# Kernel optimization log

Hardware: AMD Instinct MI355X
Metric: run time of the kernel (lower is better)

## Reference

```python
import jax, jax.numpy as jnp
import numpy as np

THRESH = 0.85

def setup_inputs() -> dict:
    key = jax.random.key(0)
    k1, k2 = jax.random.split(key)
    bs, d, r, c = 4, 16, 64, 64
    n = r * c
    seg = jax.random.normal(k1, (bs, d, r, c), dtype=jnp.float32)
    W = jax.random.uniform(k2, (bs, n, n), dtype=jnp.float32)
    return {"seg": seg, "W": W}

def reference(seg, W):
    bs, d, r, c = seg.shape
    # threshold affinity: keep values > 0.85
    Wt = jnp.where(W > THRESH, W, jnp.zeros((), W.dtype))
    # row-normalize: D = diag(1/rowsum(Wt)) @ Wt  (broadcast division)
    D = Wt / Wt.sum(axis=-1, keepdims=True)          # [bs, n, n]
    seg_flat = seg.reshape(bs, d, r * c)             # [bs, d, n]
    # seg_flat @ D^T : out[b,d,m] = sum_n seg[b,d,n] * D[b,m,n]
    out = jnp.einsum('bdn,bmn->bdm', seg_flat, D)
    return out.reshape(bs, d, r, c)
```

## Files before the change

### kernel.cpp

```cpp
#include <hip/hip_runtime.h>
#include <stdint.h>


typedef float v4f __attribute__((ext_vector_type(4)));

#define N_DIM 4096
#define D_DIM 16
#define THRESH 0.85f
#define RPW 4
#define CHUNK 256
#define NCHUNK (N_DIM / CHUNK)

__global__ __launch_bounds__(256) void regu_kernel(
    const float* __restrict__ seg,
    const float* __restrict__ W,
    float* __restrict__ out)
{
    __shared__ float stile[2][D_DIM * CHUNK];

    const int lane = threadIdx.x & 63;
    const int wv   = threadIdx.x >> 6;
    const int row0 = blockIdx.x * 16 + wv * RPW;
    const int b  = row0 >> 12;
    const int m0 = row0 & (N_DIM - 1);

    const float* Wp   = W   + ((size_t)b * N_DIM + m0) * N_DIM + lane * 4;
    const float* segb = seg + (size_t)b * D_DIM * N_DIM;

    float acc[RPW * D_DIM];
    float rowsum[RPW] = {0.f, 0.f, 0.f, 0.f};
#pragma unroll
    for (int i = 0; i < RPW * D_DIM; ++i) acc[i] = 0.f;

#define STAGE(c, sb)                                                          \
    do {                                                                      \
        _Pragma("unroll")                                                     \
        for (int j = 0; j < 4; ++j) {                                         \
            const int d_ = wv * 4 + j;                                        \
            const float* g_ = segb + (size_t)d_ * N_DIM + (size_t)(c) * CHUNK + lane * 4; \
            __builtin_amdgcn_global_load_lds(                                 \
                (const __attribute__((address_space(1))) uint32_t*)g_,        \
                (__attribute__((address_space(3))) uint32_t*)&stile[sb][d_ * CHUNK], \
                16, 0, 0);                                                    \
        }                                                                     \
    } while (0)

#define LOADW(dst, c)                                                         \
    do {                                                                      \
        const float* p_ = Wp + (size_t)(c) * CHUNK;                           \
        _Pragma("unroll")                                                     \
        for (int r = 0; r < RPW; ++r)                                         \
            dst[r] = __builtin_nontemporal_load(                              \
                (const v4f*)(p_ + (size_t)r * N_DIM));                        \
    } while (0)

    v4f wR0[RPW], wR1[RPW];

    auto compute = [&](const v4f (&w_in)[RPW], const int sb) {
        v4f w[RPW];
#pragma unroll
        for (int r = 0; r < RPW; ++r) {
            v4f v = w_in[r];
            v.x = (v.x > THRESH) ? v.x : 0.f;
            v.y = (v.y > THRESH) ? v.y : 0.f;
            v.z = (v.z > THRESH) ? v.z : 0.f;
            v.w = (v.w > THRESH) ? v.w : 0.f;
            w[r] = v;
            rowsum[r] += (v.x + v.y) + (v.z + v.w);
        }
#pragma unroll
        for (int d = 0; d < D_DIM; ++d) {
            const v4f s = *(const v4f*)&stile[sb][d * CHUNK + lane * 4];
#pragma unroll
            for (int r = 0; r < RPW; ++r) {
                acc[r * D_DIM + d] += w[r].x * s.x;
                acc[r * D_DIM + d] += w[r].y * s.y;
                acc[r * D_DIM + d] += w[r].z * s.z;
                acc[r * D_DIM + d] += w[r].w * s.w;
            }
        }
    };

    STAGE(0, 0);
    asm volatile("" ::: "memory");
    LOADW(wR0, 0);
    LOADW(wR1, 1);
    asm volatile("" ::: "memory");

#define PHASE_BODY(c_, WSET, SB)                                       \
    do {                                                               \
        if (c_ == 0)                                                   \
            asm volatile("s_waitcnt vmcnt(8)" ::: "memory");           \
        else if (c_ < NCHUNK - 1)                                      \
            asm volatile("s_waitcnt vmcnt(4)" ::: "memory");           \
        else                                                           \
            asm volatile("s_waitcnt vmcnt(0)" ::: "memory");           \
        __builtin_amdgcn_s_barrier();                                  \
        if (c_ + 1 < NCHUNK) STAGE(c_ + 1, (SB) ^ 1);                  \
        asm volatile("" ::: "memory");   \
        compute(WSET, SB);                                             \
        if (c_ + 2 < NCHUNK) LOADW(WSET, c_ + 2);                      \
    } while (0)

    for (int cc = 0; cc < NCHUNK; cc += 2) {
        PHASE_BODY(cc,     wR0, 0);
        PHASE_BODY(cc + 1, wR1, 1);
    }

#undef PHASE_BODY
#undef LOADW
#undef STAGE

#pragma unroll
    for (int k = 0; k < 6; ++k) {
        const int S = 32 >> k;
        const bool up = (lane >> k) & 1;
#pragma unroll
        for (int j = 0; j < S; ++j) {
            const float mine = up ? acc[j + S] : acc[j];
            const float send = up ? acc[j] : acc[j + S];
            acc[j] = mine + __shfl_xor(send, 1 << k, 64);
        }
    }

#pragma unroll
    for (int r = 0; r < RPW; ++r) {
        float s = rowsum[r];
#pragma unroll
        for (int off = 1; off < 64; off <<= 1) s += __shfl_xor(s, off, 64);
        rowsum[r] = s;
    }

    const int j = __brev((unsigned)lane) >> 26;
    const int r = j >> 4;
    const int d = j & 15;
    const float inv = 1.0f / (r < 2 ? (r == 0 ? rowsum[0] : rowsum[1])
                                    : (r == 2 ? rowsum[2] : rowsum[3]));
    out[((size_t)b * D_DIM + d) * N_DIM + (m0 + r)] = acc[0] * inv;
}

extern "C" void kernel_launch(void* const* d_in, const int* in_sizes, int n_in,
                              void* d_out, int out_size, void* d_ws, size_t ws_size,
                              hipStream_t stream) {
    const float* seg = (const float*)d_in[0];
    const float* W   = (const float*)d_in[1];
    float* out = (float*)d_out;

    regu_kernel<<<1024, 256, 0, stream>>>(seg, W, out);
}
```

Baseline: 381.9 us.

## Load seg directly into registers instead of staging through LDS

Drops the shared-memory double buffer for seg and its per-chunk barriers. Each wave now reads its 16 seg vectors per chunk straight from global memory into registers, relying on L1/L2 to serve the same data to all waves. The W prefetch is restructured into an A/B register ping-pong with a scheduling barrier. This trades block-level synchronization and LDS traffic for four times more global seg loads and higher register pressure, with only one W chunk in flight ahead.

```diff
diff --git a/kernel.cpp b/kernel.cpp
--- a/kernel.cpp
+++ b/kernel.cpp
@@ -16,8 +16,6 @@
     const float* __restrict__ W,
     float* __restrict__ out)
 {
-    __shared__ float stile[2][D_DIM * CHUNK];
-
     const int lane = threadIdx.x & 63;
     const int wv   = threadIdx.x >> 6;
     const int row0 = blockIdx.x * 16 + wv * RPW;
@@ -25,25 +23,12 @@
     const int m0 = row0 & (N_DIM - 1);
 
     const float* Wp   = W   + ((size_t)b * N_DIM + m0) * N_DIM + lane * 4;
-    const float* segb = seg + (size_t)b * D_DIM * N_DIM;
+    const float* segp = seg + (size_t)b * D_DIM * N_DIM + lane * 4;
 
     float acc[RPW * D_DIM];
     float rowsum[RPW] = {0.f, 0.f, 0.f, 0.f};
 #pragma unroll
     for (int i = 0; i < RPW * D_DIM; ++i) acc[i] = 0.f;
-
-#define STAGE(c, sb)                                                          \
-    do {                                                                      \
-        _Pragma("unroll")                                                     \
-        for (int j = 0; j < 4; ++j) {                                         \
-            const int d_ = wv * 4 + j;                                        \
-            const float* g_ = segb + (size_t)d_ * N_DIM + (size_t)(c) * CHUNK + lane * 4; \
-            __builtin_amdgcn_global_load_lds(                                 \
-                (const __attribute__((address_space(1))) uint32_t*)g_,        \
-                (__attribute__((address_space(3))) uint32_t*)&stile[sb][d_ * CHUNK], \
-                16, 0, 0);                                                    \
-        }                                                                     \
-    } while (0)
 
 #define LOADW(dst, c)                                                         \
     do {                                                                      \
@@ -54,62 +39,62 @@
                 (const v4f*)(p_ + (size_t)r * N_DIM));                        \
     } while (0)
 
-    v4f wR0[RPW], wR1[RPW];
-
-    auto compute = [&](const v4f (&w_in)[RPW], const int sb) {
-        v4f w[RPW];
-#pragma unroll
-        for (int r = 0; r < RPW; ++r) {
-            v4f v = w_in[r];
-            v.x = (v.x > THRESH) ? v.x : 0.f;
-            v.y = (v.y > THRESH) ? v.y : 0.f;
-            v.z = (v.z > THRESH) ? v.z : 0.f;
-            v.w = (v.w > THRESH) ? v.w : 0.f;
-            w[r] = v;
-            rowsum[r] += (v.x + v.y) + (v.z + v.w);
-        }
-#pragma unroll
-        for (int d = 0; d < D_DIM; ++d) {
-            const v4f s = *(const v4f*)&stile[sb][d * CHUNK + lane * 4];
-#pragma unroll
-            for (int r = 0; r < RPW; ++r) {
-                acc[r * D_DIM + d] += w[r].x * s.x;
-                acc[r * D_DIM + d] += w[r].y * s.y;
-                acc[r * D_DIM + d] += w[r].z * s.z;
-                acc[r * D_DIM + d] += w[r].w * s.w;
-            }
-        }
-    };
-
-    STAGE(0, 0);
-    asm volatile("" ::: "memory");
-    LOADW(wR0, 0);
-    LOADW(wR1, 1);
-    asm volatile("" ::: "memory");
-
-#define PHASE_BODY(c_, WSET, SB)                                       \
-    do {                                                               \
-        if (c_ == 0)                                                   \
-            asm volatile("s_waitcnt vmcnt(8)" ::: "memory");           \
-        else if (c_ < NCHUNK - 1)                                      \
-            asm volatile("s_waitcnt vmcnt(4)" ::: "memory");           \
-        else                                                           \
-            asm volatile("s_waitcnt vmcnt(0)" ::: "memory");           \
-        __builtin_amdgcn_s_barrier();                                  \
-        if (c_ + 1 < NCHUNK) STAGE(c_ + 1, (SB) ^ 1);                  \
-        asm volatile("" ::: "memory");   \
-        compute(WSET, SB);                                             \
-        if (c_ + 2 < NCHUNK) LOADW(WSET, c_ + 2);                      \
+#define SEGLOAD(s_, c)                                                        \
+    do {                                                                      \
+        _Pragma("unroll")                                                     \
+        for (int d = 0; d < D_DIM; ++d)                                       \
+            s_[d] = *(const v4f*)(segp + (size_t)d * N_DIM + (size_t)(c) * CHUNK); \
     } while (0)
 
+#define FMA_CHUNK(win, s_)                                                    \
+    do {                                                                      \
+        v4f w_[RPW];                                                          \
+        _Pragma("unroll")                                                     \
+        for (int r = 0; r < RPW; ++r) {                                       \
+            v4f v = win[r];                                                   \
+            v.x = (v.x > THRESH) ? v.x : 0.f;                                 \
+            v.y = (v.y > THRESH) ? v.y : 0.f;                                 \
+            v.z = (v.z > THRESH) ? v.z : 0.f;                                 \
+            v.w = (v.w > THRESH) ? v.w : 0.f;                                 \
+            w_[r] = v;                                                        \
+            rowsum[r] += (v.x + v.y) + (v.z + v.w);                           \
+        }                                                                     \
+        _Pragma("unroll")                                                     \
+        for (int d = 0; d < D_DIM; ++d) {                                     \
+            const v4f sv = s_[d];                                             \
+            _Pragma("unroll")                                                 \
+            for (int r = 0; r < RPW; ++r) {                                   \
+                acc[r * D_DIM + d] += w_[r].x * sv.x;                         \
+                acc[r * D_DIM + d] += w_[r].y * sv.y;                         \
+                acc[r * D_DIM + d] += w_[r].z * sv.z;                         \
+                acc[r * D_DIM + d] += w_[r].w * sv.w;                         \
+            }                                                                 \
+        }                                                                     \
+    } while (0)
+
+    v4f wA[RPW], wB[RPW];
+    LOADW(wA, 0);
+
     for (int cc = 0; cc < NCHUNK; cc += 2) {
-        PHASE_BODY(cc,     wR0, 0);
-        PHASE_BODY(cc + 1, wR1, 1);
+        {
+            v4f s[D_DIM];
+            SEGLOAD(s, cc);
+            __builtin_amdgcn_sched_barrier(0);
+            LOADW(wB, cc + 1);
+            FMA_CHUNK(wA, s);
+        }
+        {
+            v4f s[D_DIM];
+            SEGLOAD(s, cc + 1);
+            __builtin_amdgcn_sched_barrier(0);
+            if (cc + 2 < NCHUNK) LOADW(wA, cc + 2);
+            FMA_CHUNK(wB, s);
+        }
     }
 
-#undef PHASE_BODY
+#undef FMA_CHUNK
+#undef SEGLOAD
 #undef LOADW
-#undef STAGE
 
 #pragma unroll
     for (int k = 0; k < 6; ++k) {
```

Result: faster. 373.7 us (-2.1%).
